# Kernel optimization log

Measured on AMD Instinct MI355X. Metric: run time of the kernel, lower is better.

The kernel has to match this reference:

```python
import jax, jax.numpy as jnp
import numpy as np
from jax import lax

PAD_IDX = 0  # padding_index from init
B, T, E, H, V = 128, 24, 512, 512, 10000


def setup_inputs() -> dict:
    key = jax.random.key(0)
    ks = jax.random.split(key, 10)
    return {
        "images": jax.random.normal(ks[0], (B, H), jnp.float32),
        "captions": jax.random.randint(ks[1], (B, T), 0, V),
        "captions_length": jax.random.randint(ks[2], (B,), 1, T + 1),
        "W_emb": jax.random.normal(ks[3], (V, E), jnp.float32) * 0.02,
        "W_ih": jax.random.normal(ks[4], (4 * H, E), jnp.float32) * 0.02,
        "W_hh": jax.random.normal(ks[5], (4 * H, H), jnp.float32) * 0.02,
        "b_ih": jax.random.normal(ks[6], (4 * H,), jnp.float32) * 0.02,
        "b_hh": jax.random.normal(ks[7], (4 * H,), jnp.float32) * 0.02,
        "W_out": jax.random.normal(ks[8], (V, H), jnp.float32) * 0.02,
        "b_out": jax.random.normal(ks[9], (V,), jnp.float32) * 0.02,
    }


def reference(images, captions, captions_length, W_emb, W_ih, W_hh, b_ih, b_hh, W_out, b_out):
    # embedding with padding_idx: padding row forced to zero
    emb_table = W_emb.at[PAD_IDX].set(0.0)
    x = emb_table[captions]  # [B, T, E]
    bdim = images.shape[0]
    hdim = W_hh.shape[1]
    vocab = W_out.shape[0]
    bias = b_ih + b_hh

    def step(carry, xt):
        h, c = carry
        # PyTorch LSTMCell gate order: i, f, g, o
        gates = xt @ W_ih.T + h @ W_hh.T + bias  # [B, 4H]
        i, f, g, o = jnp.split(gates, 4, axis=-1)
        c = jax.nn.sigmoid(f) * c + jax.nn.sigmoid(i) * jnp.tanh(g)
        h = jax.nn.sigmoid(o) * jnp.tanh(c)
        logits = h @ W_out.T + b_out  # [B, V]
        return (h, c), logits

    c0 = jnp.zeros((bdim, hdim), images.dtype)
    _, ys = lax.scan(step, (images, c0), jnp.transpose(x, (1, 0, 2)))  # ys: [T, B, V]

    # deterministic <SOS>-like start output: one-hot at index 1, prepended at t=0
    start = jnp.zeros((vocab,), images.dtype).at[1].set(1.0)
    outputs = jnp.concatenate(
        [jnp.broadcast_to(start, (bdim, 1, vocab)), jnp.transpose(ys, (1, 0, 2))], axis=1
    )  # [B, T+1, V]
    return outputs, captions_length - 1
```

## Files before the change

### kernel.cpp

```cpp
#include <hip/hip_runtime.h>

constexpr int B_  = 128;
constexpr int T_  = 24;
constexpr int E_  = 512;
constexpr int H_  = 512;
constexpr int V_  = 10000;
constexpr int G4  = 2048;
constexpr int TP1 = 25;

typedef __attribute__((ext_vector_type(8))) short bf16x8;
typedef __attribute__((ext_vector_type(4))) short short4v;
typedef __attribute__((ext_vector_type(4))) float f32x4;

#define MFMA_16x16x32_BF16(a, b, c) __builtin_amdgcn_mfma_f32_16x16x32_bf16((a), (b), (c), 0, 0, 0)

__device__ inline unsigned short f2bf(float f) {
    unsigned int u = __float_as_uint(f);
    unsigned int r = (u + 0x7FFFu + ((u >> 16) & 1u)) >> 16;
    return (unsigned short)r;
}

__device__ inline void gl16(const unsigned short* g, unsigned short* l) {
    __builtin_amdgcn_global_load_lds(
        (const __attribute__((address_space(1))) unsigned int*)g,
        (__attribute__((address_space(3))) unsigned int*)l, 16, 0, 0);
}

__device__ inline int swz16(int row, int lq) {
    return (((row << 2) | lq) ^ (row & 7)) << 3;
}

__global__ __launch_bounds__(256) void k_cvt_all(const float* __restrict__ Wih,
                                                 const float* __restrict__ Whh,
                                                 const float* __restrict__ Wout,
                                                 const float* __restrict__ images,
                                                 unsigned short* __restrict__ dWih,
                                                 unsigned short* __restrict__ dWhh,
                                                 unsigned short* __restrict__ dWout,
                                                 unsigned short* __restrict__ dimg,
                                                 unsigned* __restrict__ cnt) {
    int b = blockIdx.x;
    if (b == 0 && threadIdx.x < 32) cnt[threadIdx.x * 32] = 0u;
    const float* src; unsigned short* dst; int i;
    if (b < 1024)      { src = Wih;    dst = dWih;  i = b * 256 + threadIdx.x; }
    else if (b < 2048) { src = Whh;    dst = dWhh;  i = (b - 1024) * 256 + threadIdx.x; }
    else if (b < 7048) { src = Wout;   dst = dWout; i = (b - 2048) * 256 + threadIdx.x; }
    else               { src = images; dst = dimg;  i = (b - 7048) * 256 + threadIdx.x; }
    float4 v = ((const float4*)src)[i];
    short4v o;
    o[0] = (short)f2bf(v.x); o[1] = (short)f2bf(v.y);
    o[2] = (short)f2bf(v.z); o[3] = (short)f2bf(v.w);
    ((short4v*)dst)[i] = o;
}

__global__ __launch_bounds__(256) void k_embed(const float* __restrict__ Wemb,
                                               const int* __restrict__ captions,
                                               unsigned short* __restrict__ Xemb) {
    int i = blockIdx.x * 256 + threadIdx.x;
    if (i >= 3072 * 128) return;
    int row = i >> 7;
    int k4  = i & 127;
    int b = row & 127, t = row >> 7;
    int tok = captions[b * T_ + t];
    short4v o = {0, 0, 0, 0};
    if (tok > 0 && tok < V_) {
        float4 v = ((const float4*)(Wemb + (long)tok * E_))[k4];
        o[0] = (short)f2bf(v.x); o[1] = (short)f2bf(v.y);
        o[2] = (short)f2bf(v.z); o[3] = (short)f2bf(v.w);
    }
    ((short4v*)Xemb)[(long)row * 128 + k4] = o;
}

__global__ __launch_bounds__(256) void k_start(float* __restrict__ out,
                                               const int* __restrict__ cap_len) {
    int idx = blockIdx.x * 256 + threadIdx.x;
    constexpr int Q = V_ / 4;
    if (idx < B_ * Q) {
        int b = idx / Q;
        int q = idx - b * Q;
        float4 zero = {0.f, 0.f, 0.f, 0.f};
        float4 one1 = {0.f, 1.f, 0.f, 0.f};
        ((float4*)out)[(long)b * (TP1 * Q) + q] = (q == 0) ? one1 : zero;
    }
    if (idx < B_) {
        out[(size_t)B_ * TP1 * V_ + idx] = (float)(cap_len[idx] - 1);
    }
}

__global__ __launch_bounds__(256) void k_pregemm(const unsigned short* __restrict__ Xemb,
                                                 const unsigned short* __restrict__ Wih,
                                                 const float* __restrict__ bih,
                                                 const float* __restrict__ bhh,
                                                 float* __restrict__ P) {
    __shared__ unsigned short ldsA[2][4096];
    __shared__ unsigned short ldsB[2][4096];
    int bid = blockIdx.x;
    int xcd = bid & 7;
    int q   = bid >> 3;
    int MI  = xcd * 3 + (q % 3);
    int NI  = q / 3;
    int i    = threadIdx.x;
    int w = i >> 6, lane = i & 63;
    int lm = lane & 15, lq = lane >> 4;
    int wr = w >> 1, wc = w & 1;

    int mm0 = ((i >> 2) & 7) ^ ((i >> 4) & 1);
    int li  = i ^ mm0;
    const unsigned short* gA = Xemb + (size_t)(MI * 128 + (li >> 2)) * 512 + (li & 3) * 8;
    const unsigned short* gB = Wih  + (size_t)(NI * 128 + (li >> 2)) * 512 + (li & 3) * 8;
    unsigned short* lA = &ldsA[0][0] + i * 8;
    unsigned short* lB = &ldsB[0][0] + i * 8;

    auto stage = [&](int buf, int ks) {
        int go = ks * 32;
        gl16(gA + go,            lA + buf * 4096);
        gl16(gA + go + 64 * 512, lA + buf * 4096 + 2048);
        gl16(gB + go,            lB + buf * 4096);
        gl16(gB + go + 64 * 512, lB + buf * 4096 + 2048);
    };

    f32x4 acc[4][4] = {};
    stage(0, 0);
    for (int ksi = 0; ksi < 16; ksi++) {
        int cur = ksi & 1;
        if (ksi < 15) stage(cur ^ 1, ksi + 1);
        __syncthreads();
        bf16x8 af[4], bfr[4];
        #pragma unroll
        for (int mi = 0; mi < 4; mi++)
            af[mi] = *(const bf16x8*)&ldsA[cur][swz16(wr * 64 + mi * 16 + lm, lq)];
        #pragma unroll
        for (int ni = 0; ni < 4; ni++)
            bfr[ni] = *(const bf16x8*)&ldsB[cur][swz16(wc * 64 + ni * 16 + lm, lq)];
        #pragma unroll
        for (int mi = 0; mi < 4; mi++)
            #pragma unroll
            for (int ni = 0; ni < 4; ni++)
                acc[mi][ni] = MFMA_16x16x32_BF16(af[mi], bfr[ni], acc[mi][ni]);
        __syncthreads();
    }

    float bias[4];
    #pragma unroll
    for (int ni = 0; ni < 4; ni++) {
        int n = NI * 128 + wc * 64 + ni * 16 + lm;
        bias[ni] = bih[n] + bhh[n];
    }
    #pragma unroll
    for (int mi = 0; mi < 4; mi++) {
        #pragma unroll
        for (int r = 0; r < 4; r++) {
            int m = MI * 128 + wr * 64 + mi * 16 + lq * 4 + r;
            #pragma unroll
            for (int ni = 0; ni < 4; ni++) {
                int n = NI * 128 + wc * 64 + ni * 16 + lm;
                P[(size_t)m * G4 + n] = acc[mi][ni][r] + bias[ni];
            }
        }
    }
}

__global__ __launch_bounds__(256, 1) void k_lstm(const float* __restrict__ P,
                                                 const unsigned short* __restrict__ h0,
                                                 unsigned* __restrict__ hx0,
                                                 unsigned* __restrict__ hx1,
                                                 unsigned short* __restrict__ Hall,
                                                 const unsigned short* __restrict__ Whh,
                                                 unsigned* __restrict__ cnt) {
    __shared__ float part[16][4][64];
    int w    = threadIdx.x >> 6;
    int lane = threadIdx.x & 63;
    int lm = lane & 15, lq = lane >> 4;
    int MI = blockIdx.x >> 5;
    int HG = blockIdx.x & 31;
    int hcol = HG * 16 + lm;
    int ks = w * 128;
    int brow = MI * 16 + lq * 4 + w;
    unsigned* myCnt = cnt + (MI * 4 + (HG >> 3)) * 32;
    unsigned* rdCnt = cnt + (MI * 4 + w) * 32;

    bf16x8 bw[4][4];
    #pragma unroll
    for (int g = 0; g < 4; g++)
        #pragma unroll
        for (int kk = 0; kk < 4; kk++)
            bw[g][kk] = *(const bf16x8*)((const short*)Whh +
                          (size_t)(g * 512 + hcol) * 512 + ks + kk * 32 + lq * 8);

    float cp = 0.f;

    for (int t = 0; t < T_; t++) {
        const float* Pr = P + (size_t)t * B_ * G4 + (size_t)brow * G4;
        float pv0 = Pr[0 * 512 + hcol];
        float pv1 = Pr[1 * 512 + hcol];
        float pv2 = Pr[2 * 512 + hcol];
        float pv3 = Pr[3 * 512 + hcol];

        bf16x8 a[4];
        if (t == 0) {
            const unsigned short* A = h0 + (size_t)(MI * 16 + lm) * 512 + ks;
            #pragma unroll
            for (int kk = 0; kk < 4; kk++)
                a[kk] = *(const bf16x8*)(A + kk * 32 + lq * 8);
        } else {
            if (lane == 0) {
                unsigned want = (unsigned)(8 * t);
                while (__hip_atomic_load(rdCnt, __ATOMIC_RELAXED,
                                         __HIP_MEMORY_SCOPE_AGENT) < want)
                    __builtin_amdgcn_s_sleep(1);
            }
            __builtin_amdgcn_wave_barrier();
            asm volatile("" ::: "memory");
            const unsigned long long* A = (const unsigned long long*)
                (((t & 1) ? hx1 : hx0) + ((size_t)(MI * 16 + lm) * 512 + ks) / 2);
            #pragma unroll
            for (int kk = 0; kk < 4; kk++) {
                union { unsigned long long q[2]; bf16x8 v; } cv;
                cv.q[0] = __hip_atomic_load(A + kk * 8 + lq * 2,
                                            __ATOMIC_RELAXED, __HIP_MEMORY_SCOPE_AGENT);
                cv.q[1] = __hip_atomic_load(A + kk * 8 + lq * 2 + 1,
                                            __ATOMIC_RELAXED, __HIP_MEMORY_SCOPE_AGENT);
                a[kk] = cv.v;
            }
        }

        f32x4 acc[4] = {};
        #pragma unroll
        for (int kk = 0; kk < 4; kk++) {
            acc[0] = MFMA_16x16x32_BF16(a[kk], bw[0][kk], acc[0]);
            acc[1] = MFMA_16x16x32_BF16(a[kk], bw[1][kk], acc[1]);
            acc[2] = MFMA_16x16x32_BF16(a[kk], bw[2][kk], acc[2]);
            acc[3] = MFMA_16x16x32_BF16(a[kk], bw[3][kk], acc[3]);
        }

        #pragma unroll
        for (int g = 0; g < 4; g++)
            #pragma unroll
            for (int r = 0; r < 4; r++)
                part[g * 4 + r][w][lane] = acc[g][r];
        __syncthreads();

        float gi = part[0*4+w][0][lane] + part[0*4+w][1][lane] + part[0*4+w][2][lane] + part[0*4+w][3][lane] + pv0;
        float gf = part[1*4+w][0][lane] + part[1*4+w][1][lane] + part[1*4+w][2][lane] + part[1*4+w][3][lane] + pv1;
        float gg = part[2*4+w][0][lane] + part[2*4+w][1][lane] + part[2*4+w][2][lane] + part[2*4+w][3][lane] + pv2;
        float go = part[3*4+w][0][lane] + part[3*4+w][1][lane] + part[3*4+w][2][lane] + part[3*4+w][3][lane] + pv3;
        float si = 1.f / (1.f + expf(-gi));
        float sf = 1.f / (1.f + expf(-gf));
        float so = 1.f / (1.f + expf(-go));
        float cn = sf * cp + si * tanhf(gg);
        float hn = so * tanhf(cn);
        cp = cn;
        unsigned short hb = f2bf(hn);
        Hall[(size_t)t * (B_ * H_) + brow * 512 + hcol] = hb;

        if (t < T_ - 1) {
            unsigned up = ((unsigned)(unsigned short)__shfl_down((int)hb, 1) << 16) | (unsigned)hb;
            unsigned* HW = (t & 1) ? hx0 : hx1;
            if (!(lm & 1))
                __hip_atomic_store(HW + (brow * 512 + hcol) / 2, up,
                                   __ATOMIC_RELAXED, __HIP_MEMORY_SCOPE_AGENT);
            asm volatile("s_waitcnt vmcnt(0)" ::: "memory");
            __syncthreads();
            if (threadIdx.x == 0)
                __hip_atomic_fetch_add(myCnt, 1u, __ATOMIC_RELAXED,
                                       __HIP_MEMORY_SCOPE_AGENT);
            __syncthreads();
        }
    }
}

__global__ __launch_bounds__(256) void k_logits(const unsigned short* __restrict__ Hall,
                                                const unsigned short* __restrict__ Wout,
                                                const float* __restrict__ bout,
                                                float* __restrict__ out) {
    __shared__ unsigned short ldsA[2][4096];
    __shared__ unsigned short ldsB[2][4096];
    int bid = blockIdx.x;
    int xcd = bid & 7;
    int q   = bid >> 3;
    int MI  = xcd * 3 + (q % 3);
    int NI  = q / 3;
    int i    = threadIdx.x;
    int w = i >> 6, lane = i & 63;
    int lm = lane & 15, lq = lane >> 4;
    int wr = w >> 1, wc = w & 1;

    int mm0 = ((i >> 2) & 7) ^ ((i >> 4) & 1);
    int li  = i ^ mm0;
    const unsigned short* gA = Hall + (size_t)(MI * 128 + (li >> 2)) * 512 + (li & 3) * 8;
    const unsigned short* gB = Wout + (size_t)(NI * 128 + (li >> 2)) * 512 + (li & 3) * 8;
    unsigned short* lA = &ldsA[0][0] + i * 8;
    unsigned short* lB = &ldsB[0][0] + i * 8;

    auto stage = [&](int buf, int ks) {
        int go = ks * 32;
        gl16(gA + go,            lA + buf * 4096);
        gl16(gA + go + 64 * 512, lA + buf * 4096 + 2048);
        gl16(gB + go,            lB + buf * 4096);
        gl16(gB + go + 64 * 512, lB + buf * 4096 + 2048);
    };

    f32x4 acc[4][4] = {};
    stage(0, 0);
    for (int ksi = 0; ksi < 16; ksi++) {
        int cur = ksi & 1;
        if (ksi < 15) stage(cur ^ 1, ksi + 1);
        __syncthreads();
        bf16x8 af[4], bfr[4];
        #pragma unroll
        for (int mi = 0; mi < 4; mi++)
            af[mi] = *(const bf16x8*)&ldsA[cur][swz16(wr * 64 + mi * 16 + lm, lq)];
        #pragma unroll
        for (int ni = 0; ni < 4; ni++)
            bfr[ni] = *(const bf16x8*)&ldsB[cur][swz16(wc * 64 + ni * 16 + lm, lq)];
        #pragma unroll
        for (int mi = 0; mi < 4; mi++)
            #pragma unroll
            for (int ni = 0; ni < 4; ni++)
                acc[mi][ni] = MFMA_16x16x32_BF16(af[mi], bfr[ni], acc[mi][ni]);
        __syncthreads();
    }

    #pragma unroll
    for (int mi = 0; mi < 4; mi++) {
        #pragma unroll
        for (int r = 0; r < 4; r++) {
            int b = wr * 64 + mi * 16 + lq * 4 + r;
            float* orow = out + ((size_t)b * TP1 + MI + 1) * V_;
            #pragma unroll
            for (int ni = 0; ni < 4; ni++) {
                int n = NI * 128 + wc * 64 + ni * 16 + lm;
                if (n < V_) orow[n] = acc[mi][ni][r] + bout[n];
            }
        }
    }
}

extern "C" void kernel_launch(void* const* d_in, const int* in_sizes, int n_in,
                              void* d_out, int out_size, void* d_ws, size_t ws_size,
                              hipStream_t stream) {
    const float* images   = (const float*)d_in[0];
    const int*   captions = (const int*)d_in[1];
    const int*   cap_len  = (const int*)d_in[2];
    const float* Wemb     = (const float*)d_in[3];
    const float* Wih      = (const float*)d_in[4];
    const float* Whh      = (const float*)d_in[5];
    const float* bih      = (const float*)d_in[6];
    const float* bhh      = (const float*)d_in[7];
    const float* Wout     = (const float*)d_in[8];
    const float* bout     = (const float*)d_in[9];
    float* out = (float*)d_out;

    char* ws = (char*)d_ws;
    unsigned short* Wih_bf  = (unsigned short*)(ws);
    unsigned short* Whh_bf  = (unsigned short*)(ws + 2097152);
    unsigned short* Wout_bf = (unsigned short*)(ws + 4194304);
    unsigned short* Xemb    = (unsigned short*)(ws + 14548992);
    unsigned short* Hall    = (unsigned short*)(ws + 17694720);
    unsigned short* h0      = (unsigned short*)(ws + 20840448);
    unsigned*       hx0     = (unsigned*)(ws + 20971520);
    unsigned*       hx1     = (unsigned*)(ws + 21102592);
    unsigned*       cnt     = (unsigned*)(ws + 21233664);
    constexpr size_t P_OFF   = 21237760;
    constexpr size_t WS_NEED = P_OFF + 25165824;
    float* P = (ws_size >= WS_NEED) ? (float*)(ws + P_OFF) : (float*)d_out;

    k_cvt_all<<<7112, 256, 0, stream>>>(Wih, Whh, Wout, images,
                                        Wih_bf, Whh_bf, Wout_bf, h0, cnt);
    k_embed<<<1536, 256, 0, stream>>>(Wemb, captions, Xemb);

    k_pregemm<<<384, 256, 0, stream>>>(Xemb, Wih_bf, bih, bhh, P);

    k_lstm<<<256, 256, 0, stream>>>(P, h0, hx0, hx1, Hall, Whh_bf, cnt);

    k_start<<<1250, 256, 0, stream>>>(out, cap_len);

    k_logits<<<1896, 256, 0, stream>>>(Hall, Wout_bf, bout, out);
}
```

Measured before the change: 340.7 us.

## Replace LSTM counter barrier with per-block step flags and widen logits tile

The per-step cross-block sync in the LSTM kernel moves from shared atomic counters (fetch_add plus an extra __syncthreads) to per-block flags that each producer stores as t+1; consumers poll 8 flags in parallel lanes. This removes atomic contention and one block barrier per step. The logits GEMM goes from 128x128 tiles with 256 threads to 128x256 tiles with 512 threads, halving A-tile reloads and the block count. It also moves k_start ahead of the LSTM when the workspace is large enough. The workspace layout is shifted to make room for the larger flag array.

```diff
diff --git a/kernel.cpp b/kernel.cpp
--- a/kernel.cpp
+++ b/kernel.cpp
@@ -38,9 +38,9 @@
                                                  unsigned short* __restrict__ dWhh,
                                                  unsigned short* __restrict__ dWout,
                                                  unsigned short* __restrict__ dimg,
-                                                 unsigned* __restrict__ cnt) {
+                                                 unsigned* __restrict__ flg) {
     int b = blockIdx.x;
-    if (b == 0 && threadIdx.x < 32) cnt[threadIdx.x * 32] = 0u;
+    if (b == 0) flg[threadIdx.x * 32] = 0u;
     const float* src; unsigned short* dst; int i;
     if (b < 1024)      { src = Wih;    dst = dWih;  i = b * 256 + threadIdx.x; }
     else if (b < 2048) { src = Whh;    dst = dWhh;  i = (b - 1024) * 256 + threadIdx.x; }
@@ -166,7 +166,7 @@
                                                  unsigned* __restrict__ hx1,
                                                  unsigned short* __restrict__ Hall,
                                                  const unsigned short* __restrict__ Whh,
-                                                 unsigned* __restrict__ cnt) {
+                                                 unsigned* __restrict__ flg) {
     __shared__ float part[16][4][64];
     int w    = threadIdx.x >> 6;
     int lane = threadIdx.x & 63;
@@ -176,8 +176,8 @@
     int hcol = HG * 16 + lm;
     int ks = w * 128;
     int brow = MI * 16 + lq * 4 + w;
-    unsigned* myCnt = cnt + (MI * 4 + (HG >> 3)) * 32;
-    unsigned* rdCnt = cnt + (MI * 4 + w) * 32;
+    unsigned* myFlg = flg + (MI * 32 + HG) * 32;
+    unsigned* wFlg  = flg + (MI * 32 + (w << 3)) * 32;
 
     bf16x8 bw[4][4];
     #pragma unroll
@@ -203,9 +203,9 @@
             for (int kk = 0; kk < 4; kk++)
                 a[kk] = *(const bf16x8*)(A + kk * 32 + lq * 8);
         } else {
-            if (lane == 0) {
-                unsigned want = (unsigned)(8 * t);
-                while (__hip_atomic_load(rdCnt, __ATOMIC_RELAXED,
+            if (lane < 8) {
+                unsigned want = (unsigned)t;
+                while (__hip_atomic_load(wFlg + lane * 32, __ATOMIC_RELAXED,
                                          __HIP_MEMORY_SCOPE_AGENT) < want)
                     __builtin_amdgcn_s_sleep(1);
             }
@@ -262,19 +262,18 @@
             asm volatile("s_waitcnt vmcnt(0)" ::: "memory");
             __syncthreads();
             if (threadIdx.x == 0)
-                __hip_atomic_fetch_add(myCnt, 1u, __ATOMIC_RELAXED,
-                                       __HIP_MEMORY_SCOPE_AGENT);
-            __syncthreads();
-        }
-    }
-}
-
-__global__ __launch_bounds__(256) void k_logits(const unsigned short* __restrict__ Hall,
+                __hip_atomic_store(myFlg, (unsigned)(t + 1), __ATOMIC_RELAXED,
+                                   __HIP_MEMORY_SCOPE_AGENT);
+        }
+    }
+}
+
+__global__ __launch_bounds__(512) void k_logits(const unsigned short* __restrict__ Hall,
                                                 const unsigned short* __restrict__ Wout,
                                                 const float* __restrict__ bout,
                                                 float* __restrict__ out) {
     __shared__ unsigned short ldsA[2][4096];
-    __shared__ unsigned short ldsB[2][4096];
+    __shared__ unsigned short ldsB[2][8192];
     int bid = blockIdx.x;
     int xcd = bid & 7;
     int q   = bid >> 3;
@@ -283,21 +282,20 @@
     int i    = threadIdx.x;
     int w = i >> 6, lane = i & 63;
     int lm = lane & 15, lq = lane >> 4;
-    int wr = w >> 1, wc = w & 1;
+    int wr = w >> 2, wc = w & 3;
 
     int mm0 = ((i >> 2) & 7) ^ ((i >> 4) & 1);
     int li  = i ^ mm0;
     const unsigned short* gA = Hall + (size_t)(MI * 128 + (li >> 2)) * 512 + (li & 3) * 8;
-    const unsigned short* gB = Wout + (size_t)(NI * 128 + (li >> 2)) * 512 + (li & 3) * 8;
+    const unsigned short* gB = Wout + (size_t)(NI * 256 + (li >> 2)) * 512 + (li & 3) * 8;
     unsigned short* lA = &ldsA[0][0] + i * 8;
     unsigned short* lB = &ldsB[0][0] + i * 8;
 
     auto stage = [&](int buf, int ks) {
         int go = ks * 32;
-        gl16(gA + go,            lA + buf * 4096);
-        gl16(gA + go + 64 * 512, lA + buf * 4096 + 2048);
-        gl16(gB + go,            lB + buf * 4096);
-        gl16(gB + go + 64 * 512, lB + buf * 4096 + 2048);
+        gl16(gA + go,             lA + buf * 4096);
+        gl16(gB + go,             lB + buf * 8192);
+        gl16(gB + go + 128 * 512, lB + buf * 8192 + 4096);
     };
 
     f32x4 acc[4][4] = {};
@@ -329,7 +327,7 @@
             float* orow = out + ((size_t)b * TP1 + MI + 1) * V_;
             #pragma unroll
             for (int ni = 0; ni < 4; ni++) {
-                int n = NI * 128 + wc * 64 + ni * 16 + lm;
+                int n = NI * 256 + wc * 64 + ni * 16 + lm;
                 if (n < V_) orow[n] = acc[mi][ni][r] + bout[n];
             }
         }
@@ -355,25 +353,28 @@
     unsigned short* Wih_bf  = (unsigned short*)(ws);
     unsigned short* Whh_bf  = (unsigned short*)(ws + 2097152);
     unsigned short* Wout_bf = (unsigned short*)(ws + 4194304);
-    unsigned short* Xemb    = (unsigned short*)(ws + 14548992);
-    unsigned short* Hall    = (unsigned short*)(ws + 17694720);
-    unsigned short* h0      = (unsigned short*)(ws + 20840448);
-    unsigned*       hx0     = (unsigned*)(ws + 20971520);
-    unsigned*       hx1     = (unsigned*)(ws + 21102592);
-    unsigned*       cnt     = (unsigned*)(ws + 21233664);
-    constexpr size_t P_OFF   = 21237760;
+    unsigned short* Xemb    = (unsigned short*)(ws + 14680064);
+    unsigned short* Hall    = (unsigned short*)(ws + 17825792);
+    unsigned short* h0      = (unsigned short*)(ws + 20971520);
+    unsigned*       hx0     = (unsigned*)(ws + 21102592);
+    unsigned*       hx1     = (unsigned*)(ws + 21233664);
+    unsigned*       flg     = (unsigned*)(ws + 21364736);
+    constexpr size_t P_OFF   = 21397504;
     constexpr size_t WS_NEED = P_OFF + 25165824;
-    float* P = (ws_size >= WS_NEED) ? (float*)(ws + P_OFF) : (float*)d_out;
+    bool ws_ok = (ws_size >= WS_NEED);
+    float* P = ws_ok ? (float*)(ws + P_OFF) : (float*)d_out;
 
     k_cvt_all<<<7112, 256, 0, stream>>>(Wih, Whh, Wout, images,
-                                        Wih_bf, Whh_bf, Wout_bf, h0, cnt);
+                                        Wih_bf, Whh_bf, Wout_bf, h0, flg);
     k_embed<<<1536, 256, 0, stream>>>(Wemb, captions, Xemb);
 
     k_pregemm<<<384, 256, 0, stream>>>(Xemb, Wih_bf, bih, bhh, P);
 
-    k_lstm<<<256, 256, 0, stream>>>(P, h0, hx0, hx1, Hall, Whh_bf, cnt);
-
-    k_start<<<1250, 256, 0, stream>>>(out, cap_len);
-
-    k_logits<<<1896, 256, 0, stream>>>(Hall, Wout_bf, bout, out);
-}
+    if (ws_ok) k_start<<<1250, 256, 0, stream>>>(out, cap_len);
+
+    k_lstm<<<256, 256, 0, stream>>>(P, h0, hx0, hx1, Hall, Whh_bf, flg);
+
+    if (!ws_ok) k_start<<<1250, 256, 0, stream>>>(out, cap_len);
+
+    k_logits<<<960, 512, 0, stream>>>(Hall, Wout_bf, bout, out);
+}
```

Result: faster. 320.0 us (-6.1%).
